# Kernel tuning notes

Measured on AMD Instinct MI355X. Metric: run time of the kernel, lower is better.

The kernel has to match this reference:

```python
import jax, jax.numpy as jnp
import numpy as np
import math

H = 1024   # d_model
NH = 32    # N // 2 state size
L_LEN = 4096
DT_MIN, DT_MAX = 0.001, 0.1


def setup_inputs() -> dict:
    key = jax.random.key(0)
    k1, k2, k3, k4 = jax.random.split(key, 4)
    C = jax.random.normal(k1, (H, NH, 2), dtype=jnp.float32)  # view_as_real complex C
    log_dt = (jax.random.uniform(k2, (H,), dtype=jnp.float32)
              * (math.log(DT_MAX) - math.log(DT_MIN)) + math.log(DT_MIN))
    # log of positive real parts (original: log(|Re(eig)|) repeated over H)
    log_A_real = jnp.log(0.5 + jax.random.uniform(k3, (H, NH), dtype=jnp.float32) * NH)
    A_imag = jax.random.normal(k4, (H, NH), dtype=jnp.float32) * math.pi
    return {"C": C, "log_dt": log_dt, "log_A_real": log_A_real,
            "A_imag": A_imag, "L": L_LEN}


def reference(C, log_dt, log_A_real, A_imag, L):
    dt = jnp.exp(log_dt)                                  # [H]
    Cc = C[..., 0] + 1j * C[..., 1]                       # [H, N] complex64
    A = -jnp.exp(log_A_real) - 1j * A_imag                # [H, N]
    dtA = A * dt[:, None]                                 # [H, N]
    # Vandermonde: exp(dtA)^l for l in [0, L)
    K = dtA[:, :, None] * jnp.arange(L, dtype=jnp.float32)  # [H, N, L]
    Cc = Cc * (jnp.exp(dtA) - 1.0) / A                    # [H, N]
    K = 2.0 * jnp.einsum('hn,hnl->hl', Cc, jnp.exp(K)).real  # [H, L]
    return K
```

## Files before the change

### kernel.cpp

```cpp
#include <hip/hip_runtime.h>
#include <math.h>


#define HH 1024
#define NH 32
#define LL 4096
#define BLOCK 256
#define CHUNK 8
#define LTILE (BLOCK * CHUNK)
#define NBLK_PER_H (LL / LTILE)

#define TWO_PI 6.28318530717958647692f
#define INV_TWO_PI 0.15915494309189533577f

__global__ __launch_bounds__(BLOCK) void s4_vandermonde(
    const float* __restrict__ C,
    const float* __restrict__ log_dt,
    const float* __restrict__ log_A_real,
    const float* __restrict__ A_imag,
    float* __restrict__ out)
{
    __shared__ float sCtr[NH], sCti[NH], sRe[NH], sFm[NH], sWr[NH], sWi[NH];

    const int h  = blockIdx.x >> 1;
    const int l0 = (blockIdx.x & 1) * LTILE;
    const int t  = threadIdx.x;

    if (t < NH) {
        const int n = t;
        const float dt  = __expf(log_dt[h]);
        const float Are = -__expf(log_A_real[h * NH + n]);
        const float Aim = -A_imag[h * NH + n];
        const float re = Are * dt;
        const float im = Aim * dt;
        float s1, c1;
        __sincosf(im, &s1, &c1);
        const float er1 = __expf(re);
        const float X = er1 * c1 - 1.0f;
        const float Y = er1 * s1;
        const float C0 = C[(h * NH + n) * 2 + 0];
        const float C1 = C[(h * NH + n) * 2 + 1];
        const float nr = C0 * X - C1 * Y;
        const float ni = C0 * Y + C1 * X;
        const float inv = 2.0f / (Are * Are + Aim * Aim);
        sCtr[n] = (nr * Are + ni * Aim) * inv;
        sCti[n] = (ni * Are - nr * Aim) * inv;
        sRe[n] = re;
        const float fm = im * INV_TWO_PI;
        sFm[n] = fm;
        const float reB = re * (float)BLOCK;
        const float erB = (reB < -80.0f) ? 0.0f : __expf(reB);
        float revB = fm * (float)BLOCK;
        revB -= floorf(revB);
        float sB, cB;
        __sincosf(revB * TWO_PI, &sB, &cB);
        sWr[n] = erB * cB;
        sWi[n] = erB * sB;
    }
    __syncthreads();

    float acc[CHUNK];
#pragma unroll
    for (int k = 0; k < CHUNK; ++k) acc[k] = 0.0f;

    const float lf = (float)(l0 + t);

    for (int n = 0; n < NH; ++n) {
        const float re = sRe[n];
        const float a = re * lf;
        if (a < -36.0f) continue;
        const float er = __expf(a);
        float rev = sFm[n] * lf;
        rev -= floorf(rev);
        float s, c;
        __sincosf(rev * TWO_PI, &s, &c);
        float zr = er * c;
        float zi = er * s;
        const float ctr = sCtr[n];
        const float cti = sCti[n];
        const float wr = sWr[n];
        const float wi = sWi[n];
#pragma unroll
        for (int k = 0; k < CHUNK; ++k) {
            acc[k] += ctr * zr - cti * zi;
            const float tr = zr * wr - zi * wi;
            zi = zr * wi + zi * wr;
            zr = tr;
        }
    }

    float* o = out + h * LL + l0 + t;
#pragma unroll
    for (int k = 0; k < CHUNK; ++k) o[k * BLOCK] = acc[k];
}

extern "C" void kernel_launch(void* const* d_in, const int* in_sizes, int n_in,
                              void* d_out, int out_size, void* d_ws, size_t ws_size,
                              hipStream_t stream) {
    const float* C          = (const float*)d_in[0];
    const float* log_dt     = (const float*)d_in[1];
    const float* log_A_real = (const float*)d_in[2];
    const float* A_imag     = (const float*)d_in[3];
    float* out              = (float*)d_out;

    s4_vandermonde<<<dim3(HH * NBLK_PER_H), dim3(BLOCK), 0, stream>>>(
        C, log_dt, log_A_real, A_imag, out);
}
```

Measured before the change: 103.7 us.

## Interleave block positions with stride 512 and cap recurrence steps per mode

```diff
diff --git a/kernel.cpp b/kernel.cpp
--- a/kernel.cpp
+++ b/kernel.cpp
@@ -7,8 +7,6 @@
 #define LL 4096
 #define BLOCK 256
 #define CHUNK 8
-#define LTILE (BLOCK * CHUNK)
-#define NBLK_PER_H (LL / LTILE)
 
 #define TWO_PI 6.28318530717958647692f
 #define INV_TWO_PI 0.15915494309189533577f
@@ -20,11 +18,12 @@
     const float* __restrict__ A_imag,
     float* __restrict__ out)
 {
-    __shared__ float sCtr[NH], sCti[NH], sRe[NH], sFm[NH], sWr[NH], sWi[NH];
+    __shared__ float4 sA[NH];
+    __shared__ float4 sB[NH];
 
-    const int h  = blockIdx.x >> 1;
-    const int l0 = (blockIdx.x & 1) * LTILE;
-    const int t  = threadIdx.x;
+    const int h = blockIdx.x >> 1;
+    const int b = blockIdx.x & 1;
+    const int t = threadIdx.x;
 
     if (t < NH) {
         const int n = t;
@@ -43,19 +42,22 @@
         const float nr = C0 * X - C1 * Y;
         const float ni = C0 * Y + C1 * X;
         const float inv = 2.0f / (Are * Are + Aim * Aim);
-        sCtr[n] = (nr * Are + ni * Aim) * inv;
-        sCti[n] = (ni * Are - nr * Aim) * inv;
-        sRe[n] = re;
+        const float ctr = (nr * Are + ni * Aim) * inv;
+        const float cti = (ni * Are - nr * Aim) * inv;
         const float fm = im * INV_TWO_PI;
-        sFm[n] = fm;
-        const float reB = re * (float)BLOCK;
-        const float erB = (reB < -80.0f) ? 0.0f : __expf(reB);
-        float revB = fm * (float)BLOCK;
-        revB -= floorf(revB);
-        float sB, cB;
-        __sincosf(revB * TWO_PI, &sB, &cB);
-        sWr[n] = erB * cB;
-        sWi[n] = erB * sB;
+
+        const float reS = re * 512.0f;
+        const float erS = (reS < -80.0f) ? 0.0f : __expf(reS);
+        double revd = (double)fm * 512.0;
+        revd -= floor(revd);
+        float sS, cS;
+        __sincosf((float)revd * TWO_PI, &sS, &cS);
+
+        const float kl = -40.0f / (re * 512.0f);
+        const int kcap = (kl >= 7.0f) ? 8 : ((int)kl + 1);
+
+        sA[n] = make_float4(ctr, cti, re, fm);
+        sB[n] = make_float4(erS * cS, erS * sS, __int_as_float(kcap), 0.0f);
     }
     __syncthreads();
 
@@ -63,35 +65,34 @@
 #pragma unroll
     for (int k = 0; k < CHUNK; ++k) acc[k] = 0.0f;
 
-    const float lf = (float)(l0 + t);
+    const float lf = (float)(b * 256 + t);
 
     for (int n = 0; n < NH; ++n) {
-        const float re = sRe[n];
-        const float a = re * lf;
-        if (a < -36.0f) continue;
+        const float4 A4 = sA[n];
+        const float a = A4.z * lf;
+        if (a < -40.0f) continue;
+        const float4 B4 = sB[n];
         const float er = __expf(a);
-        float rev = sFm[n] * lf;
+        float rev = A4.w * lf;
         rev -= floorf(rev);
         float s, c;
         __sincosf(rev * TWO_PI, &s, &c);
         float zr = er * c;
         float zi = er * s;
-        const float ctr = sCtr[n];
-        const float cti = sCti[n];
-        const float wr = sWr[n];
-        const float wi = sWi[n];
+        const int kcap = __float_as_int(B4.z);
 #pragma unroll
         for (int k = 0; k < CHUNK; ++k) {
-            acc[k] += ctr * zr - cti * zi;
-            const float tr = zr * wr - zi * wi;
-            zi = zr * wi + zi * wr;
+            if (k >= kcap) break;
+            acc[k] += A4.x * zr - A4.y * zi;
+            const float tr = zr * B4.x - zi * B4.y;
+            zi = zr * B4.y + zi * B4.x;
             zr = tr;
         }
     }
 
-    float* o = out + h * LL + l0 + t;
+    float* o = out + h * LL + b * 256 + t;
 #pragma unroll
-    for (int k = 0; k < CHUNK; ++k) o[k * BLOCK] = acc[k];
+    for (int k = 0; k < CHUNK; ++k) o[k * 512] = acc[k];
 }
 
 extern "C" void kernel_launch(void* const* d_in, const int* in_sizes, int n_in,
@@ -103,6 +104,6 @@
     const float* A_imag     = (const float*)d_in[3];
     float* out              = (float*)d_out;
 
-    s4_vandermonde<<<dim3(HH * NBLK_PER_H), dim3(BLOCK), 0, stream>>>(
+    s4_vandermonde<<<dim3(HH * 2), dim3(BLOCK), 0, stream>>>(
         C, log_dt, log_A_real, A_imag, out);
 }
```

New measurement: 86.18 us. 1.2x faster.
